# Optimization experiments

Measured on AMD Instinct MI355X. Metric: run time of the kernel, lower is better.

## Reference

```python
import jax, jax.numpy as jnp
import numpy as np

HEADS = 16
EPS = 1e-6


def setup_inputs() -> dict:
    key = jax.random.key(0)
    k1, k2, k3 = jax.random.split(key, 3)
    B, N, C = 4, 4096, 1024
    x = jax.random.normal(k1, (B, N, C), dtype=jnp.float32)
    w_qkv = jax.random.normal(k2, (3 * C, C), dtype=jnp.float32) * (C ** -0.5)
    w_out = jax.random.normal(k3, (C, C), dtype=jnp.float32) * (C ** -0.5)
    b_out = jnp.zeros((C,), dtype=jnp.float32)
    return {"x": x, "w_qkv": w_qkv, "w_out": w_out, "b_out": b_out}


def reference(x, w_qkv, w_out, b_out):
    B, N, C = x.shape
    H = HEADS
    D = C // H
    scale = D ** -0.25

    qkv = x @ w_qkv.T  # [B, N, 3C]
    q, k, v = jnp.split(qkv, 3, axis=-1)

    def heads(t):  # [B, N, C] -> [B, H, N, D]
        return t.reshape(B, N, H, D).transpose(0, 2, 1, 3)

    q, k, v = heads(q), heads(k), heads(v)

    feat = lambda t: jax.nn.elu(t) + 1.0
    q = feat(q) * scale
    k = feat(k) * scale

    kv = jnp.einsum('bhnd,bhne->bhde', k, v)      # [B, H, D, D]
    out = jnp.einsum('bhnd,bhde->bhne', q, kv)    # [B, H, N, D]
    k_sum = k.sum(axis=2)                          # [B, H, D]
    denom = jnp.einsum('bhnd,bhd->bhn', q, k_sum)  # [B, H, N]
    out = out / (denom[..., None] + EPS)

    out = out.transpose(0, 2, 1, 3).reshape(B, N, C)
    return out @ w_out.T + b_out
```

## Files before the change

kernel.cpp:

```cpp
#include <hip/hip_runtime.h>
#include <hip/hip_bf16.h>
#include <cmath>


typedef __bf16 bf16_t;
typedef __attribute__((ext_vector_type(8))) __bf16 bf16x8;
typedef __attribute__((ext_vector_type(4))) __bf16 bf16x4;
typedef __attribute__((ext_vector_type(4))) float f32x4;
typedef __attribute__((ext_vector_type(8))) float f32x8;

#define MFMA16(a, b, c) __builtin_amdgcn_mfma_f32_16x16x32_bf16((a), (b), (c), 0, 0, 0)

#define LDS_PITCH 72

__device__ __forceinline__ f32x4 zf4() { f32x4 z; z[0] = 0.f; z[1] = 0.f; z[2] = 0.f; z[3] = 0.f; return z; }

__device__ __forceinline__ float feat(float x) { return x > 0.f ? x + 1.f : expf(x); }

__device__ __forceinline__ void gld_lds16(const bf16_t* src, bf16_t* dst)
{
    __builtin_amdgcn_global_load_lds(
        (__attribute__((address_space(1))) void*)const_cast<bf16_t*>(src),
        (__attribute__((address_space(3))) void*)dst, 16, 0, 0);
}

template <int NR>
__device__ __forceinline__ void stage_async(const bf16_t* g, int ld, bf16_t* lds, int tid)
{
    const int w = tid >> 6, l = tid & 63;
    constexpr int CALLS = NR >> 5;
#pragma unroll
    for (int p = 0; p < CALLS; ++p) {
        const int chunk = w * CALLS + p;
        const int gidx = chunk * 64 + l;
        const int row = gidx >> 3;
        const int cp = gidx & 7;
        const int c = cp ^ (row & 7);
        gld_lds16(g + row * ld + c * 8, lds + chunk * 512);
    }
}

__device__ __forceinline__ bf16x8 read_frag_sw(const bf16_t* lds, int row, int cg)
{
    const int sw = cg ^ (row & 7);
    return *(const bf16x8*)(lds + row * 64 + sw * 8);
}

template <int NR>
__device__ __forceinline__ void stage_bf16(const bf16_t* g, int ld, bf16_t* lds, int tid)
{
#pragma unroll
    for (int p = 0; p < NR * 8 / 256; ++p) {
        const int gidx = p * 256 + tid;
        const int row = gidx >> 3;
        const int cp = gidx & 7;
        *(bf16x8*)(lds + row * LDS_PITCH + cp * 8) = *(const bf16x8*)(g + row * ld + cp * 8);
    }
}

__device__ __forceinline__ bf16x8 read_frag(const bf16_t* lds, int row, int cg)
{
    return *(const bf16x8*)(lds + row * LDS_PITCH + cg * 8);
}

__global__ __launch_bounds__(256) void cvt_kernel(const float* __restrict__ src, bf16_t* __restrict__ dst)
{
    const size_t idx = ((size_t)blockIdx.x * 256 + threadIdx.x) * 8;
    f32x8 f = *(const f32x8*)(src + idx);
    bf16x8 v;
#pragma unroll
    for (int t = 0; t < 8; ++t) v[t] = (bf16_t)f[t];
    *(bf16x8*)(dst + idx) = v;
}

template <int MODE>
__global__ __launch_bounds__(256, 2) void gemm_bt_kernel(
    const bf16_t* __restrict__ A, const bf16_t* __restrict__ B, int K,
    void* __restrict__ out0, bf16_t* __restrict__ out1, bf16_t* __restrict__ out2,
    const float* __restrict__ bias)
{
    __shared__ __align__(16) bf16_t As[128 * 64];
    __shared__ __align__(16) bf16_t Bs[128 * 64];
    const int tid = threadIdx.x;
    const int l = tid & 63, w = tid >> 6;
    const int wm = w >> 1, wn = w & 1;
    const int quad = l >> 4, r16 = l & 15;
    const int m0 = blockIdx.y * 128;
    const int n0 = blockIdx.x * 128;

    f32x4 acc[4][4];
#pragma unroll
    for (int i = 0; i < 4; ++i)
#pragma unroll
        for (int j = 0; j < 4; ++j) acc[i][j] = zf4();

    const bf16_t* Ab = A + (size_t)m0 * K;
    const bf16_t* Bb = B + (size_t)n0 * K;

    for (int k0 = 0; k0 < K; k0 += 64) {
        stage_async<128>(Ab + k0, K, As, tid);
        stage_async<128>(Bb + k0, K, Bs, tid);
        __syncthreads();
#pragma unroll
        for (int ks = 0; ks < 2; ++ks) {
            const int cg = ks * 4 + quad;
            bf16x8 af[4], bfr[4];
#pragma unroll
            for (int i = 0; i < 4; ++i) af[i] = read_frag_sw(As, wm * 64 + i * 16 + r16, cg);
#pragma unroll
            for (int j = 0; j < 4; ++j) bfr[j] = read_frag_sw(Bs, wn * 64 + j * 16 + r16, cg);
#pragma unroll
            for (int i = 0; i < 4; ++i)
#pragma unroll
                for (int j = 0; j < 4; ++j)
                    acc[i][j] = MFMA16(af[i], bfr[j], acc[i][j]);
        }
        __syncthreads();
    }

    const float scale = 0.3535533905932738f;
#pragma unroll
    for (int i = 0; i < 4; ++i) {
        const int mbase = m0 + wm * 64 + i * 16 + quad * 4;
#pragma unroll
        for (int j = 0; j < 4; ++j) {
            const int col = n0 + wn * 64 + j * 16 + r16;
            if (MODE == 1) {
                float* yp = (float*)out0;
                const float bb = bias[col];
#pragma unroll
                for (int r = 0; r < 4; ++r)
                    yp[(size_t)(mbase + r) * 1024 + col] = acc[i][j][r] + bb;
            } else {
                const int part = col >> 10;
                const int cc = col & 1023;
                const int hh = (mbase >> 12) * 16 + (cc >> 6);
                const int d = cc & 63;
                const int ntok = mbase & 4095;
                if (part == 0) {
                    bf16_t* qp = (bf16_t*)out0 + ((size_t)hh * 4096 + ntok) * 64 + d;
#pragma unroll
                    for (int r = 0; r < 4; ++r)
                        qp[(size_t)r * 64] = (bf16_t)(feat(acc[i][j][r]) * scale);
                } else {
                    bf16_t* tp = (part == 1 ? out1 : out2) + ((size_t)hh * 64 + d) * 4096 + ntok;
                    bf16x4 pk;
#pragma unroll
                    for (int r = 0; r < 4; ++r) {
                        float v = acc[i][j][r];
                        if (part == 1) v = feat(v) * scale;
                        pk[r] = (bf16_t)v;
                    }
                    *(bf16x4*)tp = pk;
                }
            }
        }
    }
}

__global__ __launch_bounds__(256, 2) void kv_partial_kernel(
    const bf16_t* __restrict__ KT, const bf16_t* __restrict__ VT, float* __restrict__ kvp)
{
    __shared__ __align__(16) bf16_t Ks[64 * LDS_PITCH];
    __shared__ __align__(16) bf16_t Vs[64 * LDS_PITCH];
    const int tid = threadIdx.x;
    const int l = tid & 63, w = tid >> 6;
    const int quad = l >> 4, r16 = l & 15;
    const int hh = blockIdx.x;
    const int ksp = blockIdx.y;
    const bf16_t* kb = KT + (size_t)hh * 64 * 4096 + ksp * 1024;
    const bf16_t* vb = VT + (size_t)hh * 64 * 4096 + ksp * 1024;

    f32x4 acc[4];
#pragma unroll
    for (int j = 0; j < 4; ++j) acc[j] = zf4();

    for (int k0 = 0; k0 < 1024; k0 += 64) {
        stage_bf16<64>(kb + k0, 4096, Ks, tid);
        stage_bf16<64>(vb + k0, 4096, Vs, tid);
        __syncthreads();
#pragma unroll
        for (int ks = 0; ks < 2; ++ks) {
            const int cg = ks * 4 + quad;
            bf16x8 af = read_frag(Ks, w * 16 + r16, cg);
#pragma unroll
            for (int j = 0; j < 4; ++j)
                acc[j] = MFMA16(af, read_frag(Vs, j * 16 + r16, cg), acc[j]);
        }
        __syncthreads();
    }

    float* ob = kvp + (size_t)(hh * 4 + ksp) * 4096;
    const int dbase = w * 16 + quad * 4;
#pragma unroll
    for (int j = 0; j < 4; ++j)
#pragma unroll
        for (int r = 0; r < 4; ++r)
            ob[(dbase + r) * 64 + j * 16 + r16] = acc[j][r];
}

__global__ __launch_bounds__(256) void ksum_kernel(const bf16_t* __restrict__ KT, float* __restrict__ ksum)
{
    const int gw = blockIdx.x * 4 + (threadIdx.x >> 6);
    const int l = threadIdx.x & 63;
    const bf16_t* row = KT + (size_t)gw * 4096;
    float s = 0.f;
#pragma unroll
    for (int i = 0; i < 8; ++i) {
        bf16x8 v = *(const bf16x8*)(row + l * 8 + i * 512);
#pragma unroll
        for (int t = 0; t < 8; ++t) s += (float)v[t];
    }
#pragma unroll
    for (int off = 32; off > 0; off >>= 1) s += __shfl_down(s, off);
    if (l == 0) ksum[gw] = s;
}

__global__ __launch_bounds__(256, 2) void attn_out_kernel(
    const bf16_t* __restrict__ Q, const float* __restrict__ kvp, const float* __restrict__ ksum,
    bf16_t* __restrict__ att)
{
    __shared__ __align__(16) bf16_t kvT[64 * LDS_PITCH];
    __shared__ __align__(16) bf16_t ksb[64];
    const int tid = threadIdx.x;
    const int l = tid & 63, w = tid >> 6;
    const int quad = l >> 4, r16 = l & 15;
    const int hh = blockIdx.x;
    const int b = hh >> 4, h = hh & 15;
    const int mt = blockIdx.y;

    {
        const int e = tid >> 2;
        const int d0 = (tid & 3) * 16;
        const float* base = kvp + (size_t)hh * 4 * 4096;
#pragma unroll
        for (int dd = 0; dd < 16; ++dd) {
            const int d = d0 + dd;
            const float s = base[d * 64 + e] + base[4096 + d * 64 + e] +
                            base[8192 + d * 64 + e] + base[12288 + d * 64 + e];
            kvT[e * LDS_PITCH + d] = (bf16_t)s;
        }
        if (tid < 64) ksb[tid] = (bf16_t)ksum[hh * 64 + tid];
    }
    __syncthreads();

    f32x4 acc[4][4];
    f32x4 dacc[4];
#pragma unroll
    for (int i = 0; i < 4; ++i) {
        dacc[i] = zf4();
#pragma unroll
        for (int j = 0; j < 4; ++j) acc[i][j] = zf4();
    }

    const int m0w = mt * 256 + w * 64;
    const bf16_t* qb = Q + (size_t)hh * 4096 * 64;
#pragma unroll
    for (int ks = 0; ks < 2; ++ks) {
        bf16x8 kf = *(const bf16x8*)(ksb + ks * 32 + quad * 8);
        if (r16 != 0) {
#pragma unroll
            for (int t = 0; t < 8; ++t) kf[t] = (bf16_t)0.f;
        }
        bf16x8 bfr[4];
#pragma unroll
        for (int j = 0; j < 4; ++j)
            bfr[j] = *(const bf16x8*)(kvT + (j * 16 + r16) * LDS_PITCH + ks * 32 + quad * 8);
#pragma unroll
        for (int i = 0; i < 4; ++i) {
            const bf16_t* qp = qb + (size_t)(m0w + i * 16 + r16) * 64 + ks * 32 + quad * 8;
            const bf16x8 af = *(const bf16x8*)qp;
            dacc[i] = MFMA16(af, kf, dacc[i]);
#pragma unroll
            for (int j = 0; j < 4; ++j) acc[i][j] = MFMA16(af, bfr[j], acc[i][j]);
        }
    }

#pragma unroll
    for (int i = 0; i < 4; ++i) {
        float den[4];
#pragma unroll
        for (int r = 0; r < 4; ++r)
            den[r] = __shfl(dacc[i][r], l & 48) + 1e-6f;
#pragma unroll
        for (int j = 0; j < 4; ++j) {
            const size_t colb = (size_t)h * 64 + j * 16 + r16;
#pragma unroll
            for (int r = 0; r < 4; ++r) {
                const int ntok = m0w + i * 16 + quad * 4 + r;
                att[((size_t)b * 4096 + ntok) * 1024 + colb] = (bf16_t)(acc[i][j][r] / den[r]);
            }
        }
    }
}

extern "C" void kernel_launch(void* const* d_in, const int* in_sizes, int n_in,
                              void* d_out, int out_size, void* d_ws, size_t ws_size,
                              hipStream_t stream)
{
    const float* x    = (const float*)d_in[0];
    const float* wqkv = (const float*)d_in[1];
    const float* wout = (const float*)d_in[2];
    const float* bout = (const float*)d_in[3];
    float* y = (float*)d_out;

    char* ws = (char*)d_ws;
    bf16_t* xb    = (bf16_t*)ws;
    bf16_t* wqkvb = (bf16_t*)(ws + (size_t)32 * 1048576);
    bf16_t* woutb = (bf16_t*)(ws + (size_t)38 * 1048576);
    bf16_t* Q     = (bf16_t*)(ws + (size_t)40 * 1048576);
    bf16_t* KT    = (bf16_t*)(ws + (size_t)72 * 1048576);
    bf16_t* VT    = (bf16_t*)(ws + (size_t)104 * 1048576);
    float* kvp    = (float*)ws;
    float* ksum   = (float*)(ws + (size_t)4 * 1048576);
    bf16_t* att   = KT;

    cvt_kernel<<<8192, 256, 0, stream>>>(x, xb);
    cvt_kernel<<<1536, 256, 0, stream>>>(wqkv, wqkvb);
    cvt_kernel<<<512, 256, 0, stream>>>(wout, woutb);

    gemm_bt_kernel<0><<<dim3(24, 128), 256, 0, stream>>>(xb, wqkvb, 1024, Q, KT, VT, nullptr);
    kv_partial_kernel<<<dim3(64, 4), 256, 0, stream>>>(KT, VT, kvp);
    ksum_kernel<<<1024, 256, 0, stream>>>(KT, ksum);
    attn_out_kernel<<<dim3(64, 16), 256, 0, stream>>>(Q, kvp, ksum, att);
    gemm_bt_kernel<1><<<dim3(8, 128), 256, 0, stream>>>(att, woutb, 1024, y, nullptr, nullptr, bout);
}
```

Measured before the change: 343.9 us.

## Fuse key-sum into KV partial MFMA and pre-reduce KV in separate kernel

The key column sum is now computed inside the KV partial kernel by multiplying a vector of ones against the K fragments with MFMA, which removes the separate ksum pass over K. KV is stored transposed (V as A operand) so that a small new kernel can reduce the four partials into a bf16 buffer with coalesced vector loads. The attention output blocks then just copy bf16 rows into LDS instead of each one redundantly reducing fp32 partials with strided loads. The GEMM launch bound also rises to three blocks per CU, which may force register spills.

Result: faster. 326.7 us (-5.0%).

```diff
diff --git a/kernel.cpp b/kernel.cpp
--- a/kernel.cpp
+++ b/kernel.cpp
@@ -74,7 +74,7 @@
 }
 
 template <int MODE>
-__global__ __launch_bounds__(256, 2) void gemm_bt_kernel(
+__global__ __launch_bounds__(256, 3) void gemm_bt_kernel(
     const bf16_t* __restrict__ A, const bf16_t* __restrict__ B, int K,
     void* __restrict__ out0, bf16_t* __restrict__ out1, bf16_t* __restrict__ out2,
     const float* __restrict__ bias)
@@ -159,7 +159,8 @@
 }
 
 __global__ __launch_bounds__(256, 2) void kv_partial_kernel(
-    const bf16_t* __restrict__ KT, const bf16_t* __restrict__ VT, float* __restrict__ kvp)
+    const bf16_t* __restrict__ KT, const bf16_t* __restrict__ VT,
+    float* __restrict__ kvp, float* __restrict__ ksp_out)
 {
     __shared__ __align__(16) bf16_t Ks[64 * LDS_PITCH];
     __shared__ __align__(16) bf16_t Vs[64 * LDS_PITCH];
@@ -171,9 +172,13 @@
     const bf16_t* kb = KT + (size_t)hh * 64 * 4096 + ksp * 1024;
     const bf16_t* vb = VT + (size_t)hh * 64 * 4096 + ksp * 1024;
 
-    f32x4 acc[4];
-#pragma unroll
-    for (int j = 0; j < 4; ++j) acc[j] = zf4();
+    bf16x8 ones;
+#pragma unroll
+    for (int t = 0; t < 8; ++t) ones[t] = (bf16_t)1.0f;
+
+    f32x4 acc[4], accks[4];
+#pragma unroll
+    for (int j = 0; j < 4; ++j) { acc[j] = zf4(); accks[j] = zf4(); }
 
     for (int k0 = 0; k0 < 1024; k0 += 64) {
         stage_bf16<64>(kb + k0, 4096, Ks, tid);
@@ -182,42 +187,62 @@
 #pragma unroll
         for (int ks = 0; ks < 2; ++ks) {
             const int cg = ks * 4 + quad;
-            bf16x8 af = read_frag(Ks, w * 16 + r16, cg);
-#pragma unroll
-            for (int j = 0; j < 4; ++j)
-                acc[j] = MFMA16(af, read_frag(Vs, j * 16 + r16, cg), acc[j]);
+            bf16x8 af = read_frag(Vs, w * 16 + r16, cg);
+            bf16x8 bk[4];
+#pragma unroll
+            for (int j = 0; j < 4; ++j) bk[j] = read_frag(Ks, j * 16 + r16, cg);
+#pragma unroll
+            for (int j = 0; j < 4; ++j) acc[j] = MFMA16(af, bk[j], acc[j]);
+            if (w == 0) {
+#pragma unroll
+                for (int j = 0; j < 4; ++j) accks[j] = MFMA16(ones, bk[j], accks[j]);
+            }
         }
         __syncthreads();
     }
 
     float* ob = kvp + (size_t)(hh * 4 + ksp) * 4096;
-    const int dbase = w * 16 + quad * 4;
+    const int ebase = w * 16 + quad * 4;
 #pragma unroll
     for (int j = 0; j < 4; ++j)
 #pragma unroll
         for (int r = 0; r < 4; ++r)
-            ob[(dbase + r) * 64 + j * 16 + r16] = acc[j][r];
-}
-
-__global__ __launch_bounds__(256) void ksum_kernel(const bf16_t* __restrict__ KT, float* __restrict__ ksum)
-{
-    const int gw = blockIdx.x * 4 + (threadIdx.x >> 6);
-    const int l = threadIdx.x & 63;
-    const bf16_t* row = KT + (size_t)gw * 4096;
-    float s = 0.f;
-#pragma unroll
-    for (int i = 0; i < 8; ++i) {
-        bf16x8 v = *(const bf16x8*)(row + l * 8 + i * 512);
-#pragma unroll
-        for (int t = 0; t < 8; ++t) s += (float)v[t];
-    }
-#pragma unroll
-    for (int off = 32; off > 0; off >>= 1) s += __shfl_down(s, off);
-    if (l == 0) ksum[gw] = s;
+            ob[(ebase + r) * 64 + j * 16 + r16] = acc[j][r];
+
+    if (w == 0 && quad == 0) {
+        float* kso = ksp_out + (size_t)(hh * 4 + ksp) * 64;
+#pragma unroll
+        for (int j = 0; j < 4; ++j) kso[j * 16 + r16] = accks[j][0];
+    }
+}
+
+__global__ __launch_bounds__(256) void kvfix_kernel(
+    const float* __restrict__ kvp, const float* __restrict__ ksp,
+    bf16_t* __restrict__ kvb, bf16_t* __restrict__ ksumb)
+{
+    const int hh = blockIdx.x, t = threadIdx.x;
+    const float* base = kvp + (size_t)hh * 4 * 4096;
+    const int off = t * 16;
+    bf16x8 o[2];
+#pragma unroll
+    for (int c = 0; c < 4; ++c) {
+        f32x4 s = *(const f32x4*)(base + off + c * 4);
+        s += *(const f32x4*)(base + 4096 + off + c * 4);
+        s += *(const f32x4*)(base + 8192 + off + c * 4);
+        s += *(const f32x4*)(base + 12288 + off + c * 4);
+#pragma unroll
+        for (int r = 0; r < 4; ++r) o[c >> 1][(c & 1) * 4 + r] = (bf16_t)s[r];
+    }
+    *(bf16x8*)(kvb + (size_t)hh * 4096 + off) = o[0];
+    *(bf16x8*)(kvb + (size_t)hh * 4096 + off + 8) = o[1];
+    if (t < 64) {
+        const float* kb = ksp + (size_t)hh * 4 * 64;
+        ksumb[(size_t)hh * 64 + t] = (bf16_t)(kb[t] + kb[64 + t] + kb[128 + t] + kb[192 + t]);
+    }
 }
 
 __global__ __launch_bounds__(256, 2) void attn_out_kernel(
-    const bf16_t* __restrict__ Q, const float* __restrict__ kvp, const float* __restrict__ ksum,
+    const bf16_t* __restrict__ Q, const bf16_t* __restrict__ kvb, const bf16_t* __restrict__ ksumb,
     bf16_t* __restrict__ att)
 {
     __shared__ __align__(16) bf16_t kvT[64 * LDS_PITCH];
@@ -230,17 +255,11 @@
     const int mt = blockIdx.y;
 
     {
-        const int e = tid >> 2;
-        const int d0 = (tid & 3) * 16;
-        const float* base = kvp + (size_t)hh * 4 * 4096;
-#pragma unroll
-        for (int dd = 0; dd < 16; ++dd) {
-            const int d = d0 + dd;
-            const float s = base[d * 64 + e] + base[4096 + d * 64 + e] +
-                            base[8192 + d * 64 + e] + base[12288 + d * 64 + e];
-            kvT[e * LDS_PITCH + d] = (bf16_t)s;
-        }
-        if (tid < 64) ksb[tid] = (bf16_t)ksum[hh * 64 + tid];
+        const int e = tid >> 2, d0 = (tid & 3) * 16;
+        const bf16_t* kvbh = kvb + (size_t)hh * 4096;
+        *(bf16x8*)(kvT + e * LDS_PITCH + d0)     = *(const bf16x8*)(kvbh + e * 64 + d0);
+        *(bf16x8*)(kvT + e * LDS_PITCH + d0 + 8) = *(const bf16x8*)(kvbh + e * 64 + d0 + 8);
+        if (tid < 64) ksb[tid] = ksumb[(size_t)hh * 64 + tid];
     }
     __syncthreads();
 
@@ -312,7 +331,9 @@
     bf16_t* KT    = (bf16_t*)(ws + (size_t)72 * 1048576);
     bf16_t* VT    = (bf16_t*)(ws + (size_t)104 * 1048576);
     float* kvp    = (float*)ws;
-    float* ksum   = (float*)(ws + (size_t)4 * 1048576);
+    float* ksp    = (float*)(ws + (size_t)4 * 1048576);
+    bf16_t* kvb   = (bf16_t*)(ws + (size_t)5 * 1048576);
+    bf16_t* ksumb = (bf16_t*)(ws + (size_t)6 * 1048576);
     bf16_t* att   = KT;
 
     cvt_kernel<<<8192, 256, 0, stream>>>(x, xb);
@@ -320,8 +341,8 @@
     cvt_kernel<<<512, 256, 0, stream>>>(wout, woutb);
 
     gemm_bt_kernel<0><<<dim3(24, 128), 256, 0, stream>>>(xb, wqkvb, 1024, Q, KT, VT, nullptr);
-    kv_partial_kernel<<<dim3(64, 4), 256, 0, stream>>>(KT, VT, kvp);
-    ksum_kernel<<<1024, 256, 0, stream>>>(KT, ksum);
-    attn_out_kernel<<<dim3(64, 16), 256, 0, stream>>>(Q, kvp, ksum, att);
+    kv_partial_kernel<<<dim3(64, 4), 256, 0, stream>>>(KT, VT, kvp, ksp);
+    kvfix_kernel<<<64, 256, 0, stream>>>(kvp, ksp, kvb, ksumb);
+    attn_out_kernel<<<dim3(64, 16), 256, 0, stream>>>(Q, kvb, ksumb, att);
     gemm_bt_kernel<1><<<dim3(8, 128), 256, 0, stream>>>(att, woutb, 1024, y, nullptr, nullptr, bout);
 }
```
